# Kernel optimization log

Hardware: AMD Instinct MI355X
Metric: run time of the kernel (lower is better)

The kernel has to match this reference:

```python
import math
import jax, jax.numpy as jnp
import numpy as np

D = 4096      # model dim
H = 32        # query heads
KVH = 8       # kv heads (GQA)
HD = D // H   # head dim = 128
B = 8         # batch == max_batch_size (cache returns full batch)
MAXLEN = 2048 # max_seq_len (cache length)
SEQ = 16      # new tokens this step
START = 1024  # start_pos (cache fill level)


def setup_inputs() -> dict:
    key = jax.random.key(0)
    ks = jax.random.split(key, 8)
    s = 0.02  # weight init scale
    x = jax.random.normal(ks[0], (B, SEQ, D), jnp.float32)
    wq = jax.random.normal(ks[1], (D, H * HD), jnp.float32) * s
    wk = jax.random.normal(ks[2], (D, KVH * HD), jnp.float32) * s
    wv = jax.random.normal(ks[3], (D, KVH * HD), jnp.float32) * s
    wo = jax.random.normal(ks[4], (H * HD, D), jnp.float32) * s
    # rotary tables: freqs_cis = exp(i * t * theta_j) -> (cos, sin)
    inv_freq = 1.0 / (10000.0 ** (jnp.arange(0, HD, 2, dtype=jnp.float32) / HD))  # [HD//2]
    ang = jnp.arange(MAXLEN, dtype=jnp.float32)[:, None] * inv_freq[None, :]      # [MAXLEN, HD//2]
    cos, sin = jnp.cos(ang), jnp.sin(ang)
    cache_k = jax.random.normal(ks[5], (B, MAXLEN, KVH, HD), jnp.float32)
    cache_v = jax.random.normal(ks[6], (B, MAXLEN, KVH, HD), jnp.float32)
    return dict(x=x, wq=wq, wk=wk, wv=wv, wo=wo, cos=cos, sin=sin,
                cache_k=cache_k, cache_v=cache_v, start_pos=START)


def _rotary(t, cos, sin):
    # t: [B,S,h,HD] viewed as complex pairs on last dim; cos/sin: [S, HD//2]
    tr = t.reshape(*t.shape[:-1], HD // 2, 2)
    t0, t1 = tr[..., 0], tr[..., 1]
    c = cos[None, :, None, :]
    s = sin[None, :, None, :]
    o0 = t0 * c - t1 * s
    o1 = t0 * s + t1 * c
    return jnp.stack([o0, o1], axis=-1).reshape(t.shape)


def reference(x, wq, wk, wv, wo, cos, sin, cache_k, cache_v, start_pos):
    bsz, seqlen, _ = x.shape
    q = (x @ wq).reshape(bsz, seqlen, H, HD)
    k = (x @ wk).reshape(bsz, seqlen, KVH, HD)
    v = (x @ wv).reshape(bsz, seqlen, KVH, HD)
    # rotary embedding on the current positions (fp32 like the original)
    cs = jax.lax.dynamic_slice_in_dim(cos, start_pos, seqlen, 0)
    sn = jax.lax.dynamic_slice_in_dim(sin, start_pos, seqlen, 0)
    q = _rotary(q.astype(jnp.float32), cs, sn).astype(x.dtype)
    k = _rotary(k.astype(jnp.float32), cs, sn).astype(x.dtype)
    # KV-cache update; attention runs over the full cache length
    keys = jax.lax.dynamic_update_slice(cache_k, k, (0, start_pos, 0, 0))
    vals = jax.lax.dynamic_update_slice(cache_v, v, (0, start_pos, 0, 0))
    # GQA repeat (tile-per-kv-head == jnp.repeat on head axis)
    n_rep = H // KVH
    keys = jnp.repeat(keys, n_rep, axis=2)  # [B, MAXLEN, H, HD]
    vals = jnp.repeat(vals, n_rep, axis=2)
    scores = jnp.einsum('bqhd,bkhd->bhqk', q, keys) / math.sqrt(HD)
    # pad mask from cache fill level (combine_masks with mask=None)
    valid = jnp.arange(keys.shape[1]) < start_pos + seqlen  # [MAXLEN]
    neg = jnp.asarray(-jnp.inf, scores.dtype)
    scores = jnp.where(valid[None, None, None, :], scores, neg)
    probs = jax.nn.softmax(scores.astype(jnp.float32), axis=-1).astype(q.dtype)
    out = jnp.einsum('bhqk,bkhd->bqhd', probs, vals).reshape(bsz, seqlen, H * HD)
    return out @ wo
```

## Files before the change

kernel.cpp:

```cpp
#include <hip/hip_runtime.h>
#include <math.h>
#include <stdint.h>

#define D 4096
#define H 32
#define KVH 8
#define HD 128
#define B_ 8
#define SEQ 16
#define MAXLEN 2048
#define NTOK 128
#define KSPLIT 8
#define KCH 512
#define BK 32
#define TSTEPS (KCH / BK)
#define KSA 16

typedef __attribute__((ext_vector_type(8))) short bh8;
typedef __attribute__((ext_vector_type(4))) float f32x4;
typedef _Float16 f16x2 __attribute__((ext_vector_type(2)));
typedef _Float16 f16x8 __attribute__((ext_vector_type(8)));

static __device__ __forceinline__ int imin(int a, int b) { return a < b ? a : b; }

static __device__ __forceinline__ short f2bf(float x) {
    union { float f; uint32_t u; } v; v.f = x;
    uint32_t u = v.u;
    return (short)((u + 0x7fffu + ((u >> 16) & 1u)) >> 16);
}
static __device__ __forceinline__ float bf2f(short b) {
    union { uint32_t u; float f; } v; v.u = ((uint32_t)(uint16_t)b) << 16;
    return v.f;
}

static __device__ __forceinline__ float fexp2(float x) {
#if __has_builtin(__builtin_amdgcn_exp2f)
    return __builtin_amdgcn_exp2f(x);
#else
    return exp2f(x);
#endif
}

__global__ __launch_bounds__(256) void cvt_x(const float* __restrict__ x, short* __restrict__ xp) {
    int i = blockIdx.x * 256 + threadIdx.x;
    int row = i >> 10;
    int c4 = (i & 1023) << 2;
    const float4 v = ((const float4*)x)[i];
    short4 o;
    o.x = f2bf(v.x); o.y = f2bf(v.y); o.z = f2bf(v.z); o.w = f2bf(v.w);
    *(short4*)&xp[((size_t)((c4 >> 3) * 128 + row)) * 8 + (c4 & 7)] = o;
}

__global__ __launch_bounds__(256) void gemm_mfma(const short* __restrict__ xp,
                                                 const float* __restrict__ wq,
                                                 const float* __restrict__ wk,
                                                 const float* __restrict__ wv,
                                                 short* __restrict__ Pq,
                                                 short* __restrict__ Pk,
                                                 short* __restrict__ Pv) {
    const int cbid = blockIdx.x;
    const int ks = blockIdx.y;
    const float* W; short* P; int ntot; int cb;
    if (cbid < 64)      { W = wq; P = Pq; ntot = 4096; cb = cbid * 64; }
    else if (cbid < 80) { W = wk; P = Pk; ntot = 1024; cb = (cbid - 64) * 64; }
    else                { W = wv; P = Pv; ntot = 1024; cb = (cbid - 80) * 64; }
    const int tid = threadIdx.x;
    const int lane = tid & 63;
    const int w = tid >> 6;
    const int wm = w >> 1, wn = w & 1;
    const int lrow = lane & 15, lkg = lane >> 4;
    const int k0 = ks * KCH;

    __shared__ __align__(16) short Wl[2][64][32];

    f32x4 acc[4][2];
#pragma unroll
    for (int fm = 0; fm < 4; ++fm)
#pragma unroll
        for (int fn = 0; fn < 2; ++fn) acc[fm][fn] = (f32x4){0.f, 0.f, 0.f, 0.f};

    const short* abase = xp + ((size_t)((k0 >> 3) + lkg) * 128 + wm * 64 + lrow) * 8;
    const int n4 = (tid & 15) * 4;
    const int r2 = (tid >> 4) * 2;
    const float* wbase = W + (size_t)(k0 + r2) * ntot + cb + n4;

    auto issueA = [&](int t, bh8 (&ar)[4]) {
        const short* p = abase + (size_t)t * 4096;
#pragma unroll
        for (int fm = 0; fm < 4; ++fm)
            ar[fm] = *(const bh8*)(p + fm * 128);
    };
    auto issueW = [&](int t, float4& fa, float4& fb) {
        const float* p = wbase + (size_t)t * 32 * ntot;
        fa = *(const float4*)p;
        fb = *(const float4*)(p + ntot);
    };
    auto storeW = [&](int bufw, const float4& fa, const float4& fb) {
        *(short2*)&Wl[bufw][n4 + 0][r2] = make_short2(f2bf(fa.x), f2bf(fb.x));
        *(short2*)&Wl[bufw][n4 + 1][r2] = make_short2(f2bf(fa.y), f2bf(fb.y));
        *(short2*)&Wl[bufw][n4 + 2][r2] = make_short2(f2bf(fa.z), f2bf(fb.z));
        *(short2*)&Wl[bufw][n4 + 3][r2] = make_short2(f2bf(fa.w), f2bf(fb.w));
    };
    auto compute = [&](int bufc, const bh8 (&ar)[4]) {
#pragma unroll
        for (int fn = 0; fn < 2; ++fn) {
            const bh8 bfr = *(const bh8*)&Wl[bufc][wn * 32 + fn * 16 + lrow][lkg * 8];
#pragma unroll
            for (int fm = 0; fm < 4; ++fm)
                acc[fm][fn] = __builtin_amdgcn_mfma_f32_16x16x32_bf16(ar[fm], bfr, acc[fm][fn], 0, 0, 0);
        }
    };

    bh8 arE[4], arO[4];
    float4 wEa, wEb, wOa, wOb;

    issueA(0, arE);
    issueW(0, wEa, wEb);
    issueW(1, wOa, wOb);
    storeW(0, wEa, wEb);
    asm volatile("s_waitcnt lgkmcnt(0)" ::: "memory");
    __builtin_amdgcn_s_barrier();

#pragma unroll
    for (int t = 0; t < TSTEPS; ++t) {
        if ((t & 1) == 0) {
            if (t + 1 < TSTEPS) issueA(t + 1, arO);
            if (t + 2 < TSTEPS) issueW(t + 2, wEa, wEb);
            compute(0, arE);
            if (t + 1 < TSTEPS) storeW(1, wOa, wOb);
        } else {
            if (t + 1 < TSTEPS) issueA(t + 1, arE);
            if (t + 2 < TSTEPS) issueW(t + 2, wOa, wOb);
            compute(1, arO);
            if (t + 1 < TSTEPS) storeW(0, wEa, wEb);
        }
        if (t + 1 < TSTEPS) {
            asm volatile("s_waitcnt lgkmcnt(0)" ::: "memory");
            __builtin_amdgcn_s_barrier();
        }
    }

    short* pp = P + (size_t)ks * NTOK * ntot;
#pragma unroll
    for (int fm = 0; fm < 4; ++fm) {
        const int gr0 = wm * 64 + fm * 16 + lkg * 4;
#pragma unroll
        for (int fn = 0; fn < 2; ++fn) {
            const int gc = cb + wn * 32 + fn * 16 + lrow;
#pragma unroll
            for (int q = 0; q < 4; ++q)
                pp[(size_t)(gr0 + q) * ntot + gc] = f2bf(acc[fm][fn][q]);
        }
    }
}

__global__ __launch_bounds__(256) void combine_rot(const short* __restrict__ Pq,
                                                   const short* __restrict__ Pk,
                                                   const short* __restrict__ Pv,
                                                   float* __restrict__ qb,
                                                   float* __restrict__ knb,
                                                   float* __restrict__ vnb,
                                                   const float* __restrict__ cosT,
                                                   const float* __restrict__ sinT,
                                                   const int* __restrict__ startp) {
    int gid = blockIdx.x * 256 + threadIdx.x;
    int tok = gid / 3072;
    int pr = gid % 3072;
    int col = pr * 2;
    int start = *startp;
    int pos = start + (tok & (SEQ - 1));
    float a = 0.f, b = 0.f;
    if (col < 4096) {
        const short* base = Pq + (size_t)tok * 4096 + col;
#pragma unroll
        for (int ks = 0; ks < KSPLIT; ++ks) {
            short2 t = *(const short2*)(base + (size_t)ks * NTOK * 4096);
            a += bf2f(t.x); b += bf2f(t.y);
        }
        int i = (col & 127) >> 1;
        float c = cosT[pos * 64 + i], s = sinT[pos * 64 + i];
        qb[(size_t)tok * 4096 + col]     = a * c - b * s;
        qb[(size_t)tok * 4096 + col + 1] = a * s + b * c;
    } else if (col < 5120) {
        int colr = col - 4096;
        const short* base = Pk + (size_t)tok * 1024 + colr;
#pragma unroll
        for (int ks = 0; ks < KSPLIT; ++ks) {
            short2 t = *(const short2*)(base + (size_t)ks * NTOK * 1024);
            a += bf2f(t.x); b += bf2f(t.y);
        }
        int i = (colr & 127) >> 1;
        float c = cosT[pos * 64 + i], s = sinT[pos * 64 + i];
        knb[(size_t)tok * 1024 + colr]     = a * c - b * s;
        knb[(size_t)tok * 1024 + colr + 1] = a * s + b * c;
    } else {
        int colr = col - 5120;
        const short* base = Pv + (size_t)tok * 1024 + colr;
#pragma unroll
        for (int ks = 0; ks < KSPLIT; ++ks) {
            short2 t = *(const short2*)(base + (size_t)ks * NTOK * 1024);
            a += bf2f(t.x); b += bf2f(t.y);
        }
        vnb[(size_t)tok * 1024 + colr]     = a;
        vnb[(size_t)tok * 1024 + colr + 1] = b;
    }
}

__global__ __launch_bounds__(256) void attn_fused(const float* __restrict__ qb,
                                                  const float* __restrict__ knb,
                                                  const float* __restrict__ vnb,
                                                  const float* __restrict__ ck,
                                                  const float* __restrict__ cv,
                                                  short* __restrict__ Opart,
                                                  float* __restrict__ mpart,
                                                  float* __restrict__ lpart,
                                                  const int* __restrict__ startp) {
    const int ksb = blockIdx.x;
    const int kvh = blockIdx.y;
    const int b   = blockIdx.z;
    const int start = *startp;
    const int klen = start + SEQ;
    const int chunk = (klen + KSA - 1) / KSA;
    const int bbeg = ksb * chunk;
    const int bend = imin(bbeg + chunk, klen);
    const int tiles = (chunk + 31) >> 5;

    const int tid = threadIdx.x;
    const int w = tid >> 6, lane = tid & 63;
    const int c = lane & 15, g = lane >> 4;
    const int hh = kvh * 4 + w;

    __shared__ __align__(16) _Float16 Ksh[2][16][32][8];
    __shared__ __align__(16) _Float16 Vsh[2][4][128][8];

    const float scl2 = 0.08838834764831843f * 1.4426950408889634f;

    f16x8 qfr[4];
    {
        const float* qp = qb + (size_t)(b * SEQ + c) * 4096 + hh * 128 + 8 * g;
#pragma unroll
        for (int h = 0; h < 4; ++h) {
            float4 a = *(const float4*)(qp + 32 * h);
            float4 b2 = *(const float4*)(qp + 32 * h + 4);
            qfr[h][0] = (_Float16)(a.x * scl2);  qfr[h][1] = (_Float16)(a.y * scl2);
            qfr[h][2] = (_Float16)(a.z * scl2);  qfr[h][3] = (_Float16)(a.w * scl2);
            qfr[h][4] = (_Float16)(b2.x * scl2); qfr[h][5] = (_Float16)(b2.y * scl2);
            qfr[h][6] = (_Float16)(b2.z * scl2); qfr[h][7] = (_Float16)(b2.w * scl2);
        }
    }

    f32x4 acc_o[8];
#pragma unroll
    for (int dm = 0; dm < 8; ++dm) acc_o[dm] = (f32x4){0.f, 0.f, 0.f, 0.f};
    float mrun = -INFINITY, lrun = 0.f;

    const int s_   = tid & 31;
    const int dgA  = tid >> 5;
    const int koffK = 8 * ((s_ >> 2) & 3) + 4 * (s_ >> 4) + (s_ & 3);
    const int kg0 = tid >> 6, d0 = (tid & 63) * 2;

    float4 kr0, kr1, kr2, kr3;
    float2 vrw[8];
    auto gloadRaw = [&](int t) {
        const int kp = bbeg + t * 32 + koffK;
        kr0 = (float4){0.f,0.f,0.f,0.f}; kr1 = kr0; kr2 = kr0; kr3 = kr0;
        if (kp < bend) {
            const float* kr = (kp < start)
                ? ck + ((size_t)((b * MAXLEN + kp) * KVH + kvh)) * HD
                : knb + (size_t)(b * SEQ + kp - start) * 1024 + kvh * HD;
            kr0 = *(const float4*)(kr + dgA * 8);
            kr1 = *(const float4*)(kr + dgA * 8 + 4);
            kr2 = *(const float4*)(kr + dgA * 8 + 64);
            kr3 = *(const float4*)(kr + dgA * 8 + 68);
        }
#pragma unroll
        for (int j = 0; j < 8; ++j) {
            const int kpv = bbeg + t * 32 + kg0 * 8 + j;
            vrw[j] = (float2){0.f, 0.f};
            if (kpv < bend) {
                const float* vrp = (kpv < start)
                    ? cv + ((size_t)((b * MAXLEN + kpv) * KVH + kvh)) * HD + d0
                    : vnb + (size_t)(b * SEQ + kpv - start) * 1024 + kvh * HD + d0;
                vrw[j] = *(const float2*)vrp;
            }
        }
    };
    auto cvtStore = [&](int bf) {
        f16x8 ka, kb;
        ka[0]=(_Float16)kr0.x; ka[1]=(_Float16)kr0.y; ka[2]=(_Float16)kr0.z; ka[3]=(_Float16)kr0.w;
        ka[4]=(_Float16)kr1.x; ka[5]=(_Float16)kr1.y; ka[6]=(_Float16)kr1.z; ka[7]=(_Float16)kr1.w;
        kb[0]=(_Float16)kr2.x; kb[1]=(_Float16)kr2.y; kb[2]=(_Float16)kr2.z; kb[3]=(_Float16)kr2.w;
        kb[4]=(_Float16)kr3.x; kb[5]=(_Float16)kr3.y; kb[6]=(_Float16)kr3.z; kb[7]=(_Float16)kr3.w;
        *(f16x8*)&Ksh[bf][dgA][s_][0] = ka;
        *(f16x8*)&Ksh[bf][dgA + 8][s_][0] = kb;
        f16x8 w0, w1;
#pragma unroll
        for (int j = 0; j < 8; ++j) { w0[j] = (_Float16)vrw[j].x; w1[j] = (_Float16)vrw[j].y; }
        *(f16x8*)&Vsh[bf][kg0][d0][0] = w0;
        *(f16x8*)&Vsh[bf][kg0][d0 + 1][0] = w1;
    };

    gloadRaw(0);
    cvtStore(0);
    __syncthreads();

    int buf = 0;
    for (int t = 0; t < tiles; ++t) {
        if (t + 1 < tiles) gloadRaw(t + 1);
        const int nk = imin(32, bend - (bbeg + t * 32));

        f32x4 acc_s[2];
        acc_s[0] = (f32x4){0.f, 0.f, 0.f, 0.f};
        acc_s[1] = (f32x4){0.f, 0.f, 0.f, 0.f};
#pragma unroll
        for (int h = 0; h < 4; ++h) {
#pragma unroll
            for (int m = 0; m < 2; ++m) {
                const f16x8 afr = *(const f16x8*)&Ksh[buf][h * 4 + g][m * 16 + c][0];
                acc_s[m] = __builtin_amdgcn_mfma_f32_16x16x32_f16(afr, qfr[h], acc_s[m], 0, 0, 0);
            }
        }
        float s8[8];
#pragma unroll
        for (int m = 0; m < 2; ++m)
#pragma unroll
            for (int q = 0; q < 4; ++q) s8[m * 4 + q] = acc_s[m][q];
        if (nk < 32) {
#pragma unroll
            for (int jj = 0; jj < 8; ++jj)
                if (8 * g + jj >= nk) s8[jj] = -1e30f;
        }
        float tmax = s8[0];
#pragma unroll
        for (int jj = 1; jj < 8; ++jj) tmax = fmaxf(tmax, s8[jj]);
        tmax = fmaxf(tmax, __shfl_xor(tmax, 16));
        tmax = fmaxf(tmax, __shfl_xor(tmax, 32));
        if (__any(tmax > mrun + 11.5f)) {
            const float mn = fmaxf(mrun, tmax);
            const float fac = fexp2(mrun - mn);
            lrun *= fac;
#pragma unroll
            for (int dm = 0; dm < 8; ++dm) {
                acc_o[dm][0] *= fac; acc_o[dm][1] *= fac;
                acc_o[dm][2] *= fac; acc_o[dm][3] *= fac;
            }
            mrun = mn;
        }
        float pe[8];
#pragma unroll
        for (int jj = 0; jj < 8; ++jj) pe[jj] = fexp2(s8[jj] - mrun);
#pragma unroll
        for (int jj = 0; jj < 8; ++jj) lrun += pe[jj];
        f16x8 bp;
#pragma unroll
        for (int jj = 0; jj < 8; ++jj) bp[jj] = (_Float16)pe[jj];

#pragma unroll
        for (int dm = 0; dm < 8; ++dm) {
            const f16x8 av = *(const f16x8*)&Vsh[buf][g][dm * 16 + c][0];
            acc_o[dm] = __builtin_amdgcn_mfma_f32_16x16x32_f16(av, bp, acc_o[dm], 0, 0, 0);
        }

        if (t + 1 < tiles) cvtStore(buf ^ 1);
        __syncthreads();
        buf ^= 1;
    }

    lrun += __shfl_xor(lrun, 16);
    lrun += __shfl_xor(lrun, 32);

    const int base = ((b * KVH + kvh) * KSA + ksb) * 64;
    const int row = w * 16 + c;
#pragma unroll
    for (int dm = 0; dm < 8; ++dm) {
        short4 o4;
        o4.x = f2bf(acc_o[dm][0]); o4.y = f2bf(acc_o[dm][1]);
        o4.z = f2bf(acc_o[dm][2]); o4.w = f2bf(acc_o[dm][3]);
        *(short4*)&Opart[(size_t)(base + row) * 128 + dm * 16 + g * 4] = o4;
    }
    if (g == 0) { mpart[base + row] = mrun; lpart[base + row] = lrun; }
}

__global__ __launch_bounds__(256) void attn_merge(const short* __restrict__ Opart,
                                                  const float* __restrict__ mpart,
                                                  const float* __restrict__ lpart,
                                                  short* __restrict__ aob) {
    const int bkvh = blockIdx.x;
    const int tid = threadIdx.x;
    __shared__ float sf[KSA][64];
    __shared__ float sinvL[64];
    if (tid < 64) {
        const int row = tid;
        float M = -INFINITY;
#pragma unroll
        for (int ks = 0; ks < KSA; ++ks)
            M = fmaxf(M, mpart[(size_t)(bkvh * KSA + ks) * 64 + row]);
        float L = 0.f;
#pragma unroll
        for (int ks = 0; ks < KSA; ++ks) {
            float f = exp2f(mpart[(size_t)(bkvh * KSA + ks) * 64 + row] - M);
            sf[ks][row] = f;
            L += f * lpart[(size_t)(bkvh * KSA + ks) * 64 + row];
        }
        sinvL[row] = 1.f / L;
    }
    __syncthreads();
    const int b = bkvh >> 3, kvh = bkvh & 7;
    for (int e = tid; e < 2048; e += 256) {
        const int row = e >> 5;
        const int d4 = (e & 31) << 2;
        float a0 = 0.f, a1 = 0.f, a2 = 0.f, a3 = 0.f;
#pragma unroll
        for (int ks = 0; ks < KSA; ++ks) {
            const short4 sp = *(const short4*)&Opart[((size_t)(bkvh * KSA + ks) * 64 + row) * 128 + d4];
            const float f = sf[ks][row];
            a0 = fmaf(f, bf2f(sp.x), a0);
            a1 = fmaf(f, bf2f(sp.y), a1);
            a2 = fmaf(f, bf2f(sp.z), a2);
            a3 = fmaf(f, bf2f(sp.w), a3);
        }
        const float iL = sinvL[row];
        a0 *= iL; a1 *= iL; a2 *= iL; a3 *= iL;
        const int hh = kvh * 4 + (row >> 4);
        const int tok = b * SEQ + (row & 15);
        const int col = hh * 128 + d4;
        short4 o;
        o.x = f2bf(a0); o.y = f2bf(a1); o.z = f2bf(a2); o.w = f2bf(a3);
        *(short4*)&aob[((size_t)(col >> 3) * 128 + tok) * 8 + (col & 7)] = o;
    }
}

__global__ __launch_bounds__(256) void sum_parts(const short* __restrict__ P,
                                                 float* __restrict__ out) {
    int i = blockIdx.x * 256 + threadIdx.x;
    float a0 = 0.f, a1 = 0.f, a2 = 0.f, a3 = 0.f;
#pragma unroll
    for (int ks = 0; ks < KSPLIT; ++ks) {
        const short4 t = ((const short4*)(P + (size_t)ks * NTOK * 4096))[i];
        a0 += bf2f(t.x); a1 += bf2f(t.y); a2 += bf2f(t.z); a3 += bf2f(t.w);
    }
    ((float4*)out)[i] = make_float4(a0, a1, a2, a3);
}

extern "C" void kernel_launch(void* const* d_in, const int* in_sizes, int n_in,
                              void* d_out, int out_size, void* d_ws, size_t ws_size,
                              hipStream_t stream) {
    const float* x  = (const float*)d_in[0];
    const float* wq = (const float*)d_in[1];
    const float* wk = (const float*)d_in[2];
    const float* wv = (const float*)d_in[3];
    const float* wo = (const float*)d_in[4];
    const float* cs = (const float*)d_in[5];
    const float* sn = (const float*)d_in[6];
    const float* ck = (const float*)d_in[7];
    const float* cv = (const float*)d_in[8];
    const int* startp = (const int*)d_in[9];

    short* Opart = (short*)d_ws;
    short* Pqb = Opart;
    short* Pkb = Pqb + (size_t)KSPLIT * NTOK * 4096;
    short* Pvb = Pkb + (size_t)KSPLIT * NTOK * 1024;
    float* qb   = (float*)(Opart + (size_t)64 * KSA * 64 * 128);
    float* knb  = qb + (size_t)NTOK * 4096;
    float* vnb  = knb + (size_t)NTOK * 1024;
    short* xpre = (short*)(vnb + (size_t)NTOK * 1024);
    short* aob  = xpre + (size_t)NTOK * 4096;
    float* mpart = (float*)(aob + (size_t)NTOK * 4096);
    float* lpart = mpart + (size_t)64 * KSA * 64;

    cvt_x<<<512, 256, 0, stream>>>(x, xpre);
    gemm_mfma<<<dim3(96, KSPLIT), 256, 0, stream>>>(xpre, wq, wk, wv, Pqb, Pkb, Pvb);
    combine_rot<<<1536, 256, 0, stream>>>(Pqb, Pkb, Pvb, qb, knb, vnb, cs, sn, startp);
    attn_fused<<<dim3(KSA, KVH, B_), 256, 0, stream>>>(qb, knb, vnb, ck, cv, Opart, mpart, lpart, startp);
    attn_merge<<<64, 256, 0, stream>>>(Opart, mpart, lpart, aob);
    gemm_mfma<<<dim3(64, KSPLIT), 256, 0, stream>>>(aob, wo, wo, wo, Pqb, Pqb, Pqb);
    sum_parts<<<512, 256, 0, stream>>>(Pqb, (float*)d_out);
}
```

Before: 104.1 us.

## Repack fp32 weights to bf16 MFMA-friendly layout before projection GEMMs

Adds a repack_w kernel that converts the wq/wk/wv/wo fp32 weights each call into a bf16 layout tiled for MFMA fragments, staged through shared memory, and a new gemm_pk kernel that reads those packed tiles with double-buffered register loads. The goal is contiguous, conversion-free weight loads inside the GEMM inner loop. The cost is an extra full pass over the weights on every call: the fp32 read plus the bf16 write in repack_w, followed by the bf16 read in gemm_pk. The new path runs only when the workspace is large enough, otherwise the old path runs.

```diff
diff --git a/kernel.cpp b/kernel.cpp
--- a/kernel.cpp
+++ b/kernel.cpp
@@ -49,6 +49,128 @@
     short4 o;
     o.x = f2bf(v.x); o.y = f2bf(v.y); o.z = f2bf(v.z); o.w = f2bf(v.w);
     *(short4*)&xp[((size_t)((c4 >> 3) * 128 + row)) * 8 + (c4 & 7)] = o;
+}
+
+__global__ __launch_bounds__(256) void repack_w(const float* __restrict__ W,
+                                                short* __restrict__ Pk,
+                                                int ntot) {
+    const int nchunk = ntot >> 10;
+    const int bid = blockIdx.x;
+    const int kb = bid / nchunk;
+    const int cc = (bid - kb * nchunk) << 10;
+    const int k0 = kb * 8;
+    const int tid = threadIdx.x;
+    __shared__ short Ls[8][1024];
+
+    const float* rp = W + (size_t)k0 * ntot + cc + tid * 4;
+    float4 v0 = *(const float4*)(rp);
+    float4 v1 = *(const float4*)(rp + (size_t)1 * ntot);
+    float4 v2 = *(const float4*)(rp + (size_t)2 * ntot);
+    float4 v3 = *(const float4*)(rp + (size_t)3 * ntot);
+    float4 v4 = *(const float4*)(rp + (size_t)4 * ntot);
+    float4 v5 = *(const float4*)(rp + (size_t)5 * ntot);
+    float4 v6 = *(const float4*)(rp + (size_t)6 * ntot);
+    float4 v7 = *(const float4*)(rp + (size_t)7 * ntot);
+    const int c4 = tid * 4;
+    {
+        short4 o;
+        o.x=f2bf(v0.x); o.y=f2bf(v0.y); o.z=f2bf(v0.z); o.w=f2bf(v0.w); *(short4*)&Ls[0][c4] = o;
+        o.x=f2bf(v1.x); o.y=f2bf(v1.y); o.z=f2bf(v1.z); o.w=f2bf(v1.w); *(short4*)&Ls[1][c4] = o;
+        o.x=f2bf(v2.x); o.y=f2bf(v2.y); o.z=f2bf(v2.z); o.w=f2bf(v2.w); *(short4*)&Ls[2][c4] = o;
+        o.x=f2bf(v3.x); o.y=f2bf(v3.y); o.z=f2bf(v3.z); o.w=f2bf(v3.w); *(short4*)&Ls[3][c4] = o;
+        o.x=f2bf(v4.x); o.y=f2bf(v4.y); o.z=f2bf(v4.z); o.w=f2bf(v4.w); *(short4*)&Ls[4][c4] = o;
+        o.x=f2bf(v5.x); o.y=f2bf(v5.y); o.z=f2bf(v5.z); o.w=f2bf(v5.w); *(short4*)&Ls[5][c4] = o;
+        o.x=f2bf(v6.x); o.y=f2bf(v6.y); o.z=f2bf(v6.z); o.w=f2bf(v6.w); *(short4*)&Ls[6][c4] = o;
+        o.x=f2bf(v7.x); o.y=f2bf(v7.y); o.z=f2bf(v7.z); o.w=f2bf(v7.w); *(short4*)&Ls[7][c4] = o;
+    }
+    __syncthreads();
+    const int ks = k0 >> 9;
+    const int kq = (k0 >> 3) & 63;
+#pragma unroll
+    for (int u = 0; u < 4; ++u) {
+        const int cl = c4 + u;
+        const int c = cc + cl;
+        bh8 o;
+#pragma unroll
+        for (int r = 0; r < 8; ++r) o[r] = Ls[r][cl];
+        short* dst = Pk + (size_t)((c >> 6) * KSPLIT + ks) * 32768
+                        + ((size_t)(kq * 64) + (c & 63)) * 8;
+        *(bh8*)dst = o;
+    }
+}
+
+__global__ __launch_bounds__(256) void gemm_pk(const short* __restrict__ xp,
+                                               const short* __restrict__ wpq,
+                                               const short* __restrict__ wpk,
+                                               const short* __restrict__ wpv,
+                                               short* __restrict__ Pq,
+                                               short* __restrict__ Pk,
+                                               short* __restrict__ Pv) {
+    const int cbid = blockIdx.x;
+    const int ks = blockIdx.y;
+    const short* Wp; short* P; int ntot; int cbl;
+    if (cbid < 64)      { Wp = wpq; P = Pq; ntot = 4096; cbl = cbid; }
+    else if (cbid < 80) { Wp = wpk; P = Pk; ntot = 1024; cbl = cbid - 64; }
+    else                { Wp = wpv; P = Pv; ntot = 1024; cbl = cbid - 80; }
+    const int cb = cbl * 64;
+    const int tid = threadIdx.x;
+    const int lane = tid & 63;
+    const int w = tid >> 6;
+    const int wm = w >> 1, wn = w & 1;
+    const int lrow = lane & 15, lkg = lane >> 4;
+    const int k0 = ks * KCH;
+
+    f32x4 acc[4][2];
+#pragma unroll
+    for (int fm = 0; fm < 4; ++fm)
+#pragma unroll
+        for (int fn = 0; fn < 2; ++fn) acc[fm][fn] = (f32x4){0.f, 0.f, 0.f, 0.f};
+
+    const short* abase = xp + ((size_t)((k0 >> 3) + lkg) * 128 + wm * 64 + lrow) * 8;
+    const short* wbase = Wp + (size_t)(cbl * KSPLIT + ks) * 32768
+                            + ((size_t)(lkg * 64) + wn * 32 + lrow) * 8;
+
+    auto issueA = [&](int t, bh8 (&ar)[4]) {
+        const short* p = abase + (size_t)t * 4096;
+#pragma unroll
+        for (int fm = 0; fm < 4; ++fm)
+            ar[fm] = *(const bh8*)(p + fm * 128);
+    };
+    auto issueW = [&](int t, bh8& b0, bh8& b1) {
+        const short* p = wbase + (size_t)t * 2048;
+        b0 = *(const bh8*)p;
+        b1 = *(const bh8*)(p + 128);
+    };
+    auto comp = [&](const bh8 (&ar)[4], const bh8& b0, const bh8& b1) {
+#pragma unroll
+        for (int fm = 0; fm < 4; ++fm) {
+            acc[fm][0] = __builtin_amdgcn_mfma_f32_16x16x32_bf16(ar[fm], b0, acc[fm][0], 0, 0, 0);
+            acc[fm][1] = __builtin_amdgcn_mfma_f32_16x16x32_bf16(ar[fm], b1, acc[fm][1], 0, 0, 0);
+        }
+    };
+
+    bh8 arE[4], arO[4];
+    bh8 wE0, wE1, wO0, wO1;
+    issueA(0, arE); issueW(0, wE0, wE1);
+    for (int t = 0; t < TSTEPS; t += 2) {
+        issueA(t + 1, arO); issueW(t + 1, wO0, wO1);
+        comp(arE, wE0, wE1);
+        if (t + 2 < TSTEPS) { issueA(t + 2, arE); issueW(t + 2, wE0, wE1); }
+        comp(arO, wO0, wO1);
+    }
+
+    short* pp = P + (size_t)ks * NTOK * ntot;
+#pragma unroll
+    for (int fm = 0; fm < 4; ++fm) {
+        const int gr0 = wm * 64 + fm * 16 + lkg * 4;
+#pragma unroll
+        for (int fn = 0; fn < 2; ++fn) {
+            const int gc = cb + wn * 32 + fn * 16 + lrow;
+#pragma unroll
+            for (int q = 0; q < 4; ++q)
+                pp[(size_t)(gr0 + q) * ntot + gc] = f2bf(acc[fm][fn][q]);
+        }
+    }
 }
 
 __global__ __launch_bounds__(256) void gemm_mfma(const short* __restrict__ xp,
@@ -467,12 +589,30 @@
     short* aob  = xpre + (size_t)NTOK * 4096;
     float* mpart = (float*)(aob + (size_t)NTOK * 4096);
     float* lpart = mpart + (size_t)64 * KSA * 64;
-
-    cvt_x<<<512, 256, 0, stream>>>(x, xpre);
-    gemm_mfma<<<dim3(96, KSPLIT), 256, 0, stream>>>(xpre, wq, wk, wv, Pqb, Pkb, Pvb);
-    combine_rot<<<1536, 256, 0, stream>>>(Pqb, Pkb, Pvb, qb, knb, vnb, cs, sn, startp);
-    attn_fused<<<dim3(KSA, KVH, B_), 256, 0, stream>>>(qb, knb, vnb, ck, cv, Opart, mpart, lpart, startp);
-    attn_merge<<<64, 256, 0, stream>>>(Opart, mpart, lpart, aob);
-    gemm_mfma<<<dim3(64, KSPLIT), 256, 0, stream>>>(aob, wo, wo, wo, Pqb, Pqb, Pqb);
-    sum_parts<<<512, 256, 0, stream>>>(Pqb, (float*)d_out);
-}
+    short* wqp = (short*)(lpart + (size_t)64 * KSA * 64);
+    short* wkp = wqp + (size_t)4096 * 4096;
+    short* wvp = wkp + (size_t)4096 * 1024;
+    const size_t need = (size_t)((char*)(wvp + (size_t)4096 * 1024) - (char*)d_ws);
+
+    if (ws_size >= need) {
+        repack_w<<<2048, 256, 0, stream>>>(wq, wqp, 4096);
+        repack_w<<<512,  256, 0, stream>>>(wk, wkp, 1024);
+        repack_w<<<512,  256, 0, stream>>>(wv, wvp, 1024);
+        cvt_x<<<512, 256, 0, stream>>>(x, xpre);
+        gemm_pk<<<dim3(96, KSPLIT), 256, 0, stream>>>(xpre, wqp, wkp, wvp, Pqb, Pkb, Pvb);
+        combine_rot<<<1536, 256, 0, stream>>>(Pqb, Pkb, Pvb, qb, knb, vnb, cs, sn, startp);
+        repack_w<<<2048, 256, 0, stream>>>(wo, wqp, 4096);
+        attn_fused<<<dim3(KSA, KVH, B_), 256, 0, stream>>>(qb, knb, vnb, ck, cv, Opart, mpart, lpart, startp);
+        attn_merge<<<64, 256, 0, stream>>>(Opart, mpart, lpart, aob);
+        gemm_pk<<<dim3(64, KSPLIT), 256, 0, stream>>>(aob, wqp, wqp, wqp, Pqb, Pqb, Pqb);
+        sum_parts<<<512, 256, 0, stream>>>(Pqb, (float*)d_out);
+    } else {
+        cvt_x<<<512, 256, 0, stream>>>(x, xpre);
+        gemm_mfma<<<dim3(96, KSPLIT), 256, 0, stream>>>(xpre, wq, wk, wv, Pqb, Pkb, Pvb);
+        combine_rot<<<1536, 256, 0, stream>>>(Pqb, Pkb, Pvb, qb, knb, vnb, cs, sn, startp);
+        attn_fused<<<dim3(KSA, KVH, B_), 256, 0, stream>>>(qb, knb, vnb, ck, cv, Opart, mpart, lpart, startp);
+        attn_merge<<<64, 256, 0, stream>>>(Opart, mpart, lpart, aob);
+        gemm_mfma<<<dim3(64, KSPLIT), 256, 0, stream>>>(aob, wo, wo, wo, Pqb, Pqb, Pqb);
+        sum_parts<<<512, 256, 0, stream>>>(Pqb, (float*)d_out);
+    }
+}
```

Result: slower. 155.2 us (+49.1%).
